# Performance work log

Measured on AMD Instinct MI355X. Metric: run time of the kernel, lower is better.

The kernel has to match this reference:

```python
import jax, jax.numpy as jnp
import numpy as np

NEG_INF = -1e9  # stand-in for -inf so fully-masked rows stay finite


def setup_inputs() -> dict:
    key = jax.random.key(0)
    ks = jax.random.split(key, 7)
    B, Nq, Nkv, H, D = 8, 512, 512, 16, 256
    return {
        "v_inv": jax.random.normal(ks[0], (B, Nkv, D), dtype=jnp.float32),
        "messages": jax.random.normal(ks[1], (B, Nq, Nkv, H), dtype=jnp.float32),
        "adj_matrix": jax.random.randint(ks[2], (B, Nq, Nkv), 0, 2, dtype=jnp.int32),
        "W_in": jax.random.normal(ks[3], (D, D), dtype=jnp.float32) * (1.0 / np.sqrt(D)),
        "b_in": jax.random.normal(ks[4], (D,), dtype=jnp.float32) * 0.02,
        "W_out": jax.random.normal(ks[5], (D, D), dtype=jnp.float32) * (1.0 / np.sqrt(D)),
        "b_out": jax.random.normal(ks[6], (D,), dtype=jnp.float32) * 0.02,
    }


def reference(v_inv, messages, adj_matrix, W_in, b_in, W_out, b_out):
    H = messages.shape[-1]
    D = v_inv.shape[-1]
    d_head = D // H
    # adjacency -> additive attention mask (0 where edge, -inf where not)
    attn_mask = jnp.where(adj_matrix > 0, 0.0, NEG_INF).astype(messages.dtype)
    logits = messages + attn_mask[..., None]          # [B, Nq, Nkv, H]
    attn = jax.nn.softmax(logits, axis=2)             # softmax over N_kv
    # value projection and head split
    proj = v_inv @ W_in.T + b_in                      # [B, Nkv, D]
    head_feats = proj.reshape(*proj.shape[:-1], H, d_head)  # [B, Nkv, H, dh]
    # per-head weighted aggregation of value features
    attn_out = jnp.einsum("bqkh,bkhd->bqhd", attn, head_feats)  # [B, Nq, H, dh]
    # L2 norm of attention row per head, used as a rescale
    weights = jnp.sqrt(jnp.sum(attn * attn, axis=2))  # [B, Nq, H]
    attn_out = attn_out * weights[..., None]
    attn_out = attn_out.reshape(*attn_out.shape[:-2], D)  # [B, Nq, D]
    return attn_out @ W_out.T + b_out
```

## Files before the change

### kernel.cpp

```cpp
#include <hip/hip_runtime.h>

constexpr int NQ = 512;
constexpr int NKV = 512;
constexpr int Hh = 16;
constexpr int Dd = 256;

__global__ __launch_bounds__(256) void gemm_bias(
    const float* __restrict__ A, const float* __restrict__ W,
    const float* __restrict__ bias, float* __restrict__ C) {
  __shared__ float As[64][68];
  __shared__ float Ws[64][68];
  const int t = threadIdx.x;
  const int tx = t & 15, ty = t >> 4;
  const int m0 = blockIdx.x * 64, n0 = blockIdx.y * 64;

  float acc[4][4] = {};

  for (int kb = 0; kb < 256; kb += 64) {
    __syncthreads();
#pragma unroll
    for (int i = 0; i < 4; ++i) {
      const int flat = i * 256 + t;
      const int r = flat >> 4, c4 = (flat & 15) << 2;
      const float4 av = *(const float4*)(A + (size_t)(m0 + r) * 256 + kb + c4);
      const float4 wv = *(const float4*)(W + (size_t)(n0 + r) * 256 + kb + c4);
      As[c4 + 0][r] = av.x; As[c4 + 1][r] = av.y;
      As[c4 + 2][r] = av.z; As[c4 + 3][r] = av.w;
      Ws[c4 + 0][r] = wv.x; Ws[c4 + 1][r] = wv.y;
      Ws[c4 + 2][r] = wv.z; Ws[c4 + 3][r] = wv.w;
    }
    __syncthreads();
#pragma unroll 16
    for (int k = 0; k < 64; ++k) {
      float a_[4], w_[4];
      *(float4*)a_ = *(const float4*)&As[k][ty << 2];
      *(float4*)w_ = *(const float4*)&Ws[k][tx << 2];
#pragma unroll
      for (int i = 0; i < 4; ++i)
#pragma unroll
        for (int j = 0; j < 4; ++j)
          acc[i][j] = fmaf(a_[i], w_[j], acc[i][j]);
    }
  }

  const float4 bv = *(const float4*)(bias + n0 + (tx << 2));
  const float bb[4] = {bv.x, bv.y, bv.z, bv.w};
#pragma unroll
  for (int i = 0; i < 4; ++i) {
    float4 cv;
    cv.x = acc[i][0] + bb[0]; cv.y = acc[i][1] + bb[1];
    cv.z = acc[i][2] + bb[2]; cv.w = acc[i][3] + bb[3];
    *(float4*)(C + (size_t)(m0 + (ty << 2) + i) * 256 + n0 + (tx << 2)) = cv;
  }
}

__global__ __launch_bounds__(512, 4) void attn_fused(
    const float* __restrict__ msg, const int* __restrict__ adj,
    const float* __restrict__ proj, float* __restrict__ attn_out) {
  __shared__ float Psh[4][8][256];
  __shared__ float Esh[4][8][16][12];

  const int t    = threadIdx.x;
  const int lane = t & 63;
  const int w    = t >> 6;
  const int oct  = w >> 1;
  const int qh   = w & 1;
  const int h    = lane >> 2;
  const int d4   = lane & 3;
  const int col  = lane << 2;
  const int q0   = blockIdx.x * 8;
  const int b    = blockIdx.y;

  const int p_h4  = t & 3;
  const int p_q   = (t >> 2) & 7;
  const int p_oct = (t >> 5) & 3;
  const int p_jp  = t >> 7;

  const float* mrow = msg + ((size_t)(b * NQ + q0 + p_q) * NKV) * Hh + p_h4 * 4;
  const int*   arow = adj + (size_t)(b * NQ + q0 + p_q) * NKV;
  const float* pb   = proj + (size_t)b * NKV * Dd;

  float4 o[4] = {};
  float s[4] = {}, r[4] = {};

  for (int rd = 0; rd < 16; ++rd) {
    __syncthreads();
#pragma unroll
    for (int i = 0; i < 4; ++i) {
      const int flat = i * 512 + t;
      const int row = flat >> 6;
      const int so = row >> 3, kk = row & 7;
      const int c4 = (flat & 63) << 2;
      *(float4*)&Psh[so][kk][c4] =
          *(const float4*)(pb + (size_t)(so * 128 + rd * 8 + kk) * Dd + c4);
    }
    {
      const int kg = p_oct * 128 + rd * 8 + p_jp * 2;
      const float4 mv0 = *(const float4*)(mrow + (size_t)kg * Hh);
      const float4 mv1 = *(const float4*)(mrow + (size_t)(kg + 1) * Hh);
      const int a0 = arow[kg], a1 = arow[kg + 1];
      float e0[4], e1[4];
      e0[0] = a0 > 0 ? __expf(mv0.x) : 0.f; e0[1] = a0 > 0 ? __expf(mv0.y) : 0.f;
      e0[2] = a0 > 0 ? __expf(mv0.z) : 0.f; e0[3] = a0 > 0 ? __expf(mv0.w) : 0.f;
      e1[0] = a1 > 0 ? __expf(mv1.x) : 0.f; e1[1] = a1 > 0 ? __expf(mv1.y) : 0.f;
      e1[2] = a1 > 0 ? __expf(mv1.z) : 0.f; e1[3] = a1 > 0 ? __expf(mv1.w) : 0.f;
#pragma unroll
      for (int i = 0; i < 4; ++i) {
        const int h2 = (p_h4 * 4 + i) ^ p_q;
        *(float2*)&Esh[p_oct][p_q][h2][p_jp * 2] = make_float2(e0[i], e1[i]);
      }
    }
    __syncthreads();
#pragma unroll
    for (int kh = 0; kh < 2; ++kh) {
      float4 p[4];
#pragma unroll
      for (int j = 0; j < 4; ++j)
        p[j] = *(const float4*)&Psh[oct][kh * 4 + j][col];
#pragma unroll
      for (int qi = 0; qi < 4; ++qi) {
        const int ql = qh * 4 + qi;
        const float4 e4 = *(const float4*)&Esh[oct][ql][h ^ ql][kh * 4];
        s[qi] += e4.x + e4.y + e4.z + e4.w;
        r[qi] = fmaf(e4.x, e4.x, fmaf(e4.y, e4.y,
                fmaf(e4.z, e4.z, fmaf(e4.w, e4.w, r[qi]))));
        o[qi].x = fmaf(e4.x, p[0].x, o[qi].x);
        o[qi].y = fmaf(e4.x, p[0].y, o[qi].y);
        o[qi].z = fmaf(e4.x, p[0].z, o[qi].z);
        o[qi].w = fmaf(e4.x, p[0].w, o[qi].w);
        o[qi].x = fmaf(e4.y, p[1].x, o[qi].x);
        o[qi].y = fmaf(e4.y, p[1].y, o[qi].y);
        o[qi].z = fmaf(e4.y, p[1].z, o[qi].z);
        o[qi].w = fmaf(e4.y, p[1].w, o[qi].w);
        o[qi].x = fmaf(e4.z, p[2].x, o[qi].x);
        o[qi].y = fmaf(e4.z, p[2].y, o[qi].y);
        o[qi].z = fmaf(e4.z, p[2].z, o[qi].z);
        o[qi].w = fmaf(e4.z, p[2].w, o[qi].w);
        o[qi].x = fmaf(e4.w, p[3].x, o[qi].x);
        o[qi].y = fmaf(e4.w, p[3].y, o[qi].y);
        o[qi].z = fmaf(e4.w, p[3].z, o[qi].z);
        o[qi].w = fmaf(e4.w, p[3].w, o[qi].w);
      }
    }
  }

  float4* Ro = (float4*)&Psh[0][0][0];
  float*  Rs = &Esh[0][0][0][0];
  float*  Rr = Rs + 256;

  __syncthreads();
  if (w >= 4) {
    const int reg = w - 4;
#pragma unroll
    for (int qi = 0; qi < 4; ++qi) {
      Ro[(reg * 4 + qi) * 64 + lane] = o[qi];
      if (d4 == 0) {
        Rs[(reg * 4 + qi) * 16 + h] = s[qi];
        Rr[(reg * 4 + qi) * 16 + h] = r[qi];
      }
    }
  }
  __syncthreads();
  if (w < 4) {
#pragma unroll
    for (int qi = 0; qi < 4; ++qi) {
      const float4 v = Ro[(w * 4 + qi) * 64 + lane];
      o[qi].x += v.x; o[qi].y += v.y; o[qi].z += v.z; o[qi].w += v.w;
      s[qi] += Rs[(w * 4 + qi) * 16 + h];
      r[qi] += Rr[(w * 4 + qi) * 16 + h];
    }
  }
  __syncthreads();
  if (w == 2 || w == 3) {
    const int reg = w - 2;
#pragma unroll
    for (int qi = 0; qi < 4; ++qi) {
      Ro[(reg * 4 + qi) * 64 + lane] = o[qi];
      if (d4 == 0) {
        Rs[(reg * 4 + qi) * 16 + h] = s[qi];
        Rr[(reg * 4 + qi) * 16 + h] = r[qi];
      }
    }
  }
  __syncthreads();
  if (w < 2) {
#pragma unroll
    for (int qi = 0; qi < 4; ++qi) {
      const float4 v = Ro[(w * 4 + qi) * 64 + lane];
      o[qi].x += v.x; o[qi].y += v.y; o[qi].z += v.z; o[qi].w += v.w;
      const float st = s[qi] + Rs[(w * 4 + qi) * 16 + h];
      const float rt = r[qi] + Rr[(w * 4 + qi) * 16 + h];
      const float wgt = sqrtf(rt) / (st * st);
      float4 u;
      u.x = o[qi].x * wgt; u.y = o[qi].y * wgt;
      u.z = o[qi].z * wgt; u.w = o[qi].w * wgt;
      const int q = q0 + w * 4 + qi;
      *(float4*)(attn_out + (size_t)(b * NQ + q) * Dd + col) = u;
    }
  }
}

extern "C" void kernel_launch(void* const* d_in, const int* in_sizes, int n_in,
                              void* d_out, int out_size, void* d_ws, size_t ws_size,
                              hipStream_t stream) {
  const float* v_inv    = (const float*)d_in[0];
  const float* messages = (const float*)d_in[1];
  const int*   adj      = (const int*)d_in[2];
  const float* W_in     = (const float*)d_in[3];
  const float* b_in     = (const float*)d_in[4];
  const float* W_out    = (const float*)d_in[5];
  const float* b_out    = (const float*)d_in[6];
  float* out = (float*)d_out;

  float* proj = (float*)d_ws;
  float* attn = proj + (size_t)8 * NKV * Dd;

  dim3 gg(64, 4);
  gemm_bias<<<gg, 256, 0, stream>>>(v_inv, W_in, b_in, proj);
  attn_fused<<<dim3(64, 8), 512, 0, stream>>>(messages, adj, proj, attn);
  gemm_bias<<<gg, 256, 0, stream>>>(attn, W_out, b_out, out);
}
```

Measured before the change: 260.8 us.

## Prefetch next tiles into registers and use direct global-to-LDS loads

Both GEMM and attention kernels now prefetch the next iteration's global data (A/W tiles, messages and adjacency) into registers while the current tile is computed, so memory latency overlaps with FMA work. The attention kernel also loads proj rows straight into shared memory with global_load_lds instead of staging them through registers, and raises wave priority during the compute phase. The cost is more registers in flight. The direct LDS load relies on the following barrier to make the data visible, which may be an ordering risk.

```diff
diff --git a/kernel.cpp b/kernel.cpp
--- a/kernel.cpp
+++ b/kernel.cpp
@@ -15,21 +15,36 @@
   const int m0 = blockIdx.x * 64, n0 = blockIdx.y * 64;
 
   float acc[4][4] = {};
-
-  for (int kb = 0; kb < 256; kb += 64) {
-    __syncthreads();
+  float4 av[4], wv[4];
+
+#pragma unroll
+  for (int i = 0; i < 4; ++i) {
+    const int flat = i * 256 + t;
+    const int r = flat >> 4, c4 = (flat & 15) << 2;
+    av[i] = *(const float4*)(A + (size_t)(m0 + r) * 256 + c4);
+    wv[i] = *(const float4*)(W + (size_t)(n0 + r) * 256 + c4);
+  }
+
+  for (int kb = 0; kb < 4; ++kb) {
 #pragma unroll
     for (int i = 0; i < 4; ++i) {
       const int flat = i * 256 + t;
       const int r = flat >> 4, c4 = (flat & 15) << 2;
-      const float4 av = *(const float4*)(A + (size_t)(m0 + r) * 256 + kb + c4);
-      const float4 wv = *(const float4*)(W + (size_t)(n0 + r) * 256 + kb + c4);
-      As[c4 + 0][r] = av.x; As[c4 + 1][r] = av.y;
-      As[c4 + 2][r] = av.z; As[c4 + 3][r] = av.w;
-      Ws[c4 + 0][r] = wv.x; Ws[c4 + 1][r] = wv.y;
-      Ws[c4 + 2][r] = wv.z; Ws[c4 + 3][r] = wv.w;
+      As[c4 + 0][r] = av[i].x; As[c4 + 1][r] = av[i].y;
+      As[c4 + 2][r] = av[i].z; As[c4 + 3][r] = av[i].w;
+      Ws[c4 + 0][r] = wv[i].x; Ws[c4 + 1][r] = wv[i].y;
+      Ws[c4 + 2][r] = wv[i].z; Ws[c4 + 3][r] = wv[i].w;
     }
     __syncthreads();
+    if (kb < 3) {
+#pragma unroll
+      for (int i = 0; i < 4; ++i) {
+        const int flat = i * 256 + t;
+        const int r = flat >> 4, c4 = (flat & 15) << 2;
+        av[i] = *(const float4*)(A + (size_t)(m0 + r) * 256 + (kb + 1) * 64 + c4);
+        wv[i] = *(const float4*)(W + (size_t)(n0 + r) * 256 + (kb + 1) * 64 + c4);
+      }
+    }
 #pragma unroll 16
     for (int k = 0; k < 64; ++k) {
       float a_[4], w_[4];
@@ -41,6 +56,7 @@
         for (int j = 0; j < 4; ++j)
           acc[i][j] = fmaf(a_[i], w_[j], acc[i][j]);
     }
+    if (kb < 3) __syncthreads();
   }
 
   const float4 bv = *(const float4*)(bias + n0 + (tx << 2));
@@ -83,22 +99,25 @@
   float4 o[4] = {};
   float s[4] = {}, r[4] = {};
 
+  float4 mv0, mv1;
+  int a0, a1;
+  {
+    const int kg = p_oct * 128 + p_jp * 2;
+    mv0 = *(const float4*)(mrow + (size_t)kg * Hh);
+    mv1 = *(const float4*)(mrow + (size_t)(kg + 1) * Hh);
+    a0 = arow[kg]; a1 = arow[kg + 1];
+  }
+
   for (int rd = 0; rd < 16; ++rd) {
-    __syncthreads();
 #pragma unroll
     for (int i = 0; i < 4; ++i) {
-      const int flat = i * 512 + t;
-      const int row = flat >> 6;
-      const int so = row >> 3, kk = row & 7;
-      const int c4 = (flat & 63) << 2;
-      *(float4*)&Psh[so][kk][c4] =
-          *(const float4*)(pb + (size_t)(so * 128 + rd * 8 + kk) * Dd + c4);
+      const float* g = pb + (size_t)(i * 128 + rd * 8 + w) * Dd + (lane << 2);
+      __builtin_amdgcn_global_load_lds(
+          (const __attribute__((address_space(1))) unsigned int*)g,
+          (__attribute__((address_space(3))) unsigned int*)&Psh[i][w][0],
+          16, 0, 0);
     }
     {
-      const int kg = p_oct * 128 + rd * 8 + p_jp * 2;
-      const float4 mv0 = *(const float4*)(mrow + (size_t)kg * Hh);
-      const float4 mv1 = *(const float4*)(mrow + (size_t)(kg + 1) * Hh);
-      const int a0 = arow[kg], a1 = arow[kg + 1];
       float e0[4], e1[4];
       e0[0] = a0 > 0 ? __expf(mv0.x) : 0.f; e0[1] = a0 > 0 ? __expf(mv0.y) : 0.f;
       e0[2] = a0 > 0 ? __expf(mv0.z) : 0.f; e0[3] = a0 > 0 ? __expf(mv0.w) : 0.f;
@@ -111,6 +130,15 @@
       }
     }
     __syncthreads();
+
+    if (rd < 15) {
+      const int kg = p_oct * 128 + (rd + 1) * 8 + p_jp * 2;
+      mv0 = *(const float4*)(mrow + (size_t)kg * Hh);
+      mv1 = *(const float4*)(mrow + (size_t)(kg + 1) * Hh);
+      a0 = arow[kg]; a1 = arow[kg + 1];
+    }
+
+    __builtin_amdgcn_s_setprio(1);
 #pragma unroll
     for (int kh = 0; kh < 2; ++kh) {
       float4 p[4];
@@ -142,6 +170,8 @@
         o[qi].w = fmaf(e4.w, p[3].w, o[qi].w);
       }
     }
+    __builtin_amdgcn_s_setprio(0);
+    if (rd < 15) __syncthreads();
   }
 
   float4* Ro = (float4*)&Psh[0][0][0];
```

New measurement: 251.1 us (median of 2 runs). 3.7% less time.
